# Performance work log

Measured on AMD Instinct MI355X. Metric: run time of the kernel, lower is better.

Reference implementation:

```python
import jax, jax.numpy as jnp
import numpy as np

N_POINTS = 4
HIDDEN = 128


def _grid_sample(features, grid):
    """Bilinear grid_sample, align_corners=True, zero padding.
    features: [B, C, H, W]; grid: [B, J, P, 2] with (x, y) in [-1, 1].
    Returns [B, C, J, P]."""
    B, C, H, W = features.shape
    ix = (grid[..., 0] + 1.0) * 0.5 * (W - 1)  # [B,J,P]
    iy = (grid[..., 1] + 1.0) * 0.5 * (H - 1)
    x0 = jnp.floor(ix); y0 = jnp.floor(iy)
    x1 = x0 + 1.0;      y1 = y0 + 1.0
    wx1 = ix - x0; wx0 = 1.0 - wx1
    wy1 = iy - y0; wy0 = 1.0 - wy1

    def corner(xf, yf):
        valid = (xf >= 0) & (xf <= W - 1) & (yf >= 0) & (yf <= H - 1)
        xi = jnp.clip(xf, 0, W - 1).astype(jnp.int32)
        yi = jnp.clip(yf, 0, H - 1).astype(jnp.int32)

        def gather_one(fb, yb, xb, vb):
            # fb: [C,H,W]; yb, xb, vb: [J,P]
            return fb[:, yb, xb] * vb[None].astype(fb.dtype)  # [C,J,P]

        return jax.vmap(gather_one)(features, yi, xi, valid)

    v00 = corner(x0, y0); v01 = corner(x1, y0)
    v10 = corner(x0, y1); v11 = corner(x1, y1)
    w00 = (wx0 * wy0)[:, None]  # [B,1,J,P]
    w01 = (wx1 * wy0)[:, None]
    w10 = (wx0 * wy1)[:, None]
    w11 = (wx1 * wy1)[:, None]
    return v00 * w00 + v01 * w01 + v10 * w10 + v11 * w11


def _mlp1x1(x, w1, b1, w2, b2):
    # 1x1 conv stack on [B, C, J] points: Conv(C->128) -> ReLU -> Conv(128->O)
    h = jax.nn.relu(jnp.einsum('oc,bcj->boj', w1, x) + b1[None, :, None])
    return jnp.einsum('oc,bcj->boj', w2, h) + b2[None, :, None]


def setup_inputs() -> dict:
    key = jax.random.key(0)
    ks = jax.random.split(key, 12)
    B, C, H, W, J = 32, 1024, 64, 64, 128
    features = jax.random.normal(ks[0], (B, C, H, W), dtype=jnp.float32)
    keypoint_coords = jax.random.uniform(ks[1], (B, J, 2), dtype=jnp.float32,
                                         minval=-1.0, maxval=1.0)
    # offset predictor params (small std so predicted pixel offsets stay local)
    w_off1 = jax.random.normal(ks[2], (HIDDEN, C), dtype=jnp.float32) * 0.01
    b_off1 = jax.random.normal(ks[3], (HIDDEN,), dtype=jnp.float32) * 0.01
    w_off2 = jax.random.normal(ks[4], (2 * N_POINTS, HIDDEN), dtype=jnp.float32) * 0.01
    b_off2 = jax.random.normal(ks[5], (2 * N_POINTS,), dtype=jnp.float32) * 0.01
    # attention predictor params
    w_att1 = jax.random.normal(ks[6], (HIDDEN, C), dtype=jnp.float32) * 0.02
    b_att1 = jax.random.normal(ks[7], (HIDDEN,), dtype=jnp.float32) * 0.02
    w_att2 = jax.random.normal(ks[8], (N_POINTS, HIDDEN), dtype=jnp.float32) * 0.02
    b_att2 = jax.random.normal(ks[9], (N_POINTS,), dtype=jnp.float32) * 0.02
    return {"features": features, "keypoint_coords": keypoint_coords,
            "w_off1": w_off1, "b_off1": b_off1, "w_off2": w_off2, "b_off2": b_off2,
            "w_att1": w_att1, "b_att1": b_att1, "w_att2": w_att2, "b_att2": b_att2}


def reference(features, keypoint_coords, w_off1, b_off1, w_off2, b_off2,
              w_att1, b_att1, w_att2, b_att2):
    B, C, H, W = features.shape
    J = keypoint_coords.shape[1]
    # seed features at keypoints: [B, C, J]
    seed = _grid_sample(features, keypoint_coords[:, :, None, :])[..., 0]
    offsets = _mlp1x1(seed, w_off1, b_off1, w_off2, b_off2)      # [B, 2N, J]
    attn_logits = _mlp1x1(seed, w_att1, b_att1, w_att2, b_att2)  # [B, N, J]
    # [B, 2N, J] -> [B, J, N, 2]; channel pairs are (x, y) per point
    off = offsets.transpose(0, 2, 1).reshape(B, J, N_POINTS, 2)
    scale = jnp.array([2.0 / (W - 1), 2.0 / (H - 1)], dtype=features.dtype)
    new_grid = keypoint_coords[:, :, None, :] + off * scale       # [B, J, N, 2]
    sampled = _grid_sample(features, new_grid)                    # [B, C, J, N]
    attw = jax.nn.softmax(attn_logits.transpose(0, 2, 1), axis=-1)  # [B, J, N]
    fused = jnp.einsum('bcjn,bjn->bjc', sampled, attw)            # [B, J, C]
    return fused
```

## Files before the change

kernel.cpp:

```cpp
#include <hip/hip_runtime.h>
#include <math.h>

#define BB  32
#define CCH 1024
#define HH  64
#define WW  64
#define JJ  128
#define NP  4
#define HID 128

typedef float f4 __attribute__((ext_vector_type(4)));
typedef __attribute__((ext_vector_type(8))) short bf8_t;
typedef __attribute__((ext_vector_type(4))) float f32x4;
typedef __attribute__((ext_vector_type(4))) unsigned short us4;

__device__ __forceinline__ unsigned short f2bf(float x) {
  union { float f; unsigned int u; } v; v.f = x;
  unsigned int u = v.u;
  return (unsigned short)((u + 0x7FFFu + ((u >> 16) & 1u)) >> 16);
}

__device__ __forceinline__ float bilin(const float* pl, float ix, float iy) {
  float x0f = floorf(ix), y0f = floorf(iy);
  float wx1 = ix - x0f, wx0 = 1.0f - wx1;
  float wy1 = iy - y0f, wy0 = 1.0f - wy1;
  int x0 = (int)x0f, y0 = (int)y0f;
  int x1 = x0 + 1, y1 = y0 + 1;
  float v = 0.0f;
  if (y0 >= 0 && y0 < HH) {
    if (x0 >= 0 && x0 < WW) v += pl[y0*WW + x0] * (wx0*wy0);
    if (x1 >= 0 && x1 < WW) v += pl[y0*WW + x1] * (wx1*wy0);
  }
  if (y1 >= 0 && y1 < HH) {
    if (x0 >= 0 && x0 < WW) v += pl[y1*WW + x0] * (wx0*wy1);
    if (x1 >= 0 && x1 < WW) v += pl[y1*WW + x1] * (wx1*wy1);
  }
  return v;
}

__global__ __launch_bounds__(256) void k_prep(const float* __restrict__ w_off1,
                                              const float* __restrict__ w_att1,
                                              unsigned short* __restrict__ Wb) {
  int o = blockIdx.x, m = blockIdx.y;
  const float* src = (m ? w_att1 : w_off1) + (size_t)o * CCH;
  unsigned short* dst = Wb + ((size_t)m * HID + o) * CCH;
  int t = threadIdx.x;
  f4 v = *(const f4*)&src[t * 4];
  us4 u; u[0] = f2bf(v[0]); u[1] = f2bf(v[1]); u[2] = f2bf(v[2]); u[3] = f2bf(v[3]);
  *(us4*)&dst[t * 4] = u;
}

__global__ __launch_bounds__(256) void k_seed(const float* __restrict__ feat,
                                              const float* __restrict__ kp,
                                              unsigned short* __restrict__ seedB) {
  int c = blockIdx.x, b = blockIdx.y;
  __shared__ __align__(16) float pl[HH*WW];
  const f4* p4 = (const f4*)(feat + ((size_t)(b*CCH + c)) * (size_t)(HH*WW));
  f4* s4 = (f4*)pl;
  #pragma unroll
  for (int r = 0; r < 4; ++r) s4[threadIdx.x + r*256] = p4[threadIdx.x + r*256];
  __syncthreads();
  int j = threadIdx.x;
  if (j < JJ) {
    float gx = kp[((size_t)b*JJ + j)*2 + 0];
    float gy = kp[((size_t)b*JJ + j)*2 + 1];
    float ix = (gx + 1.0f) * 0.5f * (float)(WW - 1);
    float iy = (gy + 1.0f) * 0.5f * (float)(HH - 1);
    seedB[((size_t)(b*CCH + c))*JJ + j] = f2bf(bilin(pl, ix, iy));
  }
}

__global__ __launch_bounds__(256) void k_str(const unsigned short* __restrict__ seedB,
                                             unsigned short* __restrict__ seedT) {
  int c0 = blockIdx.x * 32, j0 = blockIdx.y * 32, b = blockIdx.z;
  __shared__ unsigned short tl[32][34];
  int tx = threadIdx.x & 31, ty = threadIdx.x >> 5;
  #pragma unroll
  for (int r = 0; r < 4; ++r)
    tl[ty + r*8][tx] = seedB[((size_t)(b*CCH + c0 + ty + r*8))*JJ + j0 + tx];
  __syncthreads();
  #pragma unroll
  for (int r = 0; r < 4; ++r) {
    int jr = ty + r*8;
    seedT[((size_t)b*JJ + j0 + jr)*CCH + c0 + tx] = tl[tx][jr];
  }
}

__global__ __launch_bounds__(256) void k_mlp2(const unsigned short* __restrict__ seedT,
                                              const unsigned short* __restrict__ Wb,
                                              const float* __restrict__ b_off1,
                                              const float* __restrict__ b_att1,
                                              float* __restrict__ hidden) {
  int m = blockIdx.x, b = blockIdx.y;
  __shared__ __align__(16) unsigned short sA[128][72];
  __shared__ __align__(16) unsigned short sB[128][72];
  int t = threadIdx.x;
  int w = t >> 6, l = t & 63;
  int lr = l & 15, lg = l >> 4;
  f32x4 acc[2][8];
  #pragma unroll
  for (int jt = 0; jt < 2; ++jt)
    #pragma unroll
    for (int ot = 0; ot < 8; ++ot) acc[jt][ot] = (f32x4)0.0f;

  const unsigned short* At = seedT + (size_t)b * JJ * CCH;
  const unsigned short* Bt = Wb + (size_t)m * HID * CCH;

  for (int kc = 0; kc < 16; ++kc) {
    int k0 = kc * 64;
    #pragma unroll
    for (int q = 0; q < 4; ++q) {
      int idx = q * 256 + t;
      int r = idx >> 3, s = idx & 7;
      *(bf8_t*)&sA[r][s*8] = *(const bf8_t*)&At[(size_t)r*CCH + k0 + s*8];
      *(bf8_t*)&sB[r][s*8] = *(const bf8_t*)&Bt[(size_t)r*CCH + k0 + s*8];
    }
    __syncthreads();
    #pragma unroll
    for (int ks = 0; ks < 2; ++ks) {
      int koff = ks*32 + lg*8;
      bf8_t a0 = *(const bf8_t*)&sA[w*32 + lr][koff];
      bf8_t a1 = *(const bf8_t*)&sA[w*32 + 16 + lr][koff];
      #pragma unroll
      for (int ot = 0; ot < 8; ++ot) {
        bf8_t bb = *(const bf8_t*)&sB[ot*16 + lr][koff];
        acc[0][ot] = __builtin_amdgcn_mfma_f32_16x16x32_bf16(a0, bb, acc[0][ot], 0, 0, 0);
        acc[1][ot] = __builtin_amdgcn_mfma_f32_16x16x32_bf16(a1, bb, acc[1][ot], 0, 0, 0);
      }
    }
    __syncthreads();
  }

  const float* bias = m ? b_att1 : b_off1;
  float* Hb = hidden + ((size_t)b * 2 + m) * JJ * HID;
  #pragma unroll
  for (int jt = 0; jt < 2; ++jt) {
    #pragma unroll
    for (int ot = 0; ot < 8; ++ot) {
      int o = ot*16 + lr;
      float bo = bias[o];
      #pragma unroll
      for (int r = 0; r < 4; ++r) {
        int j = w*32 + jt*16 + lg*4 + r;
        Hb[(size_t)j*HID + o] = fmaxf(acc[jt][ot][r] + bo, 0.0f);
      }
    }
  }
}

__global__ __launch_bounds__(256) void k_head2(const float* __restrict__ hidden,
                                               const float* __restrict__ kp,
                                               const float* __restrict__ w_off2,
                                               const float* __restrict__ b_off2,
                                               const float* __restrict__ w_att2,
                                               const float* __restrict__ b_att2,
                                               float* __restrict__ grids,
                                               float* __restrict__ attw) {
  int jq = blockIdx.x, b = blockIdx.y;
  int j0 = jq * 32;
  __shared__ __align__(16) float sH[2][32][132];
  __shared__ float sO[32][13];
  int t = threadIdx.x;
  for (int idx = t; idx < 2048; idx += 256) {
    int m = idx >> 10, rem = idx & 1023;
    int jl = rem >> 5, oq = rem & 31;
    *(f4*)&sH[m][jl][oq*4] =
        *(const f4*)&hidden[(((size_t)b*2 + m)*JJ + j0 + jl)*HID + oq*4];
  }
  __syncthreads();
  for (int idx = t; idx < 12*32; idx += 256) {
    int jl = idx / 12, q = idx % 12;
    int m = (q < 8) ? 0 : 1;
    int p = m ? (q - 8) : q;
    const float* w2 = m ? w_att2 : w_off2;
    float sum = (m ? b_att2 : b_off2)[p];
    for (int o = 0; o < HID; ++o) sum += w2[p*HID + o] * sH[m][jl][o];
    sO[jl][q] = sum;
  }
  __syncthreads();
  if (t < 32) {
    int jl = t, j = j0 + jl;
    float gx = kp[((size_t)b*JJ + j)*2 + 0];
    float gy = kp[((size_t)b*JJ + j)*2 + 1];
    const float sc = 2.0f / 63.0f;
    float a[NP];
    #pragma unroll
    for (int n = 0; n < NP; ++n) {
      grids[(((size_t)b*JJ + j)*NP + n)*2 + 0] = gx + sO[jl][2*n + 0]*sc;
      grids[(((size_t)b*JJ + j)*NP + n)*2 + 1] = gy + sO[jl][2*n + 1]*sc;
      a[n] = sO[jl][8 + n];
    }
    float mx = fmaxf(fmaxf(a[0], a[1]), fmaxf(a[2], a[3]));
    float e[NP], s = 0.0f;
    #pragma unroll
    for (int n = 0; n < NP; ++n) { e[n] = expf(a[n] - mx); s += e[n]; }
    float inv = 1.0f / s;
    #pragma unroll
    for (int n = 0; n < NP; ++n) attw[((size_t)b*JJ + j)*NP + n] = e[n]*inv;
  }
}

__global__ __launch_bounds__(256) void k_fuse2(const float* __restrict__ feat,
                                               const float* __restrict__ grids,
                                               const float* __restrict__ attw,
                                               float* __restrict__ out) {
  int c0 = blockIdx.x * 16;
  int b = (BB - 1) - blockIdx.y;
  __shared__ __align__(16) float plane[2][HH*WW];
  __shared__ float sT[JJ][17];
  __shared__ float sG[JJ*NP*2];
  __shared__ float sAw[JJ*NP];
  int t = threadIdx.x;
  const f4* gb = (const f4*)(grids + (size_t)b*JJ*NP*2);
  const f4* ab = (const f4*)(attw  + (size_t)b*JJ*NP);
  ((f4*)sG)[t] = gb[t];
  if (t < 128) ((f4*)sAw)[t] = ab[t];

  const float* base = feat + ((size_t)(b*CCH + c0)) * (size_t)(HH*WW);
  f4 r[4];
  {
    const f4* p0 = (const f4*)base;
    #pragma unroll
    for (int q = 0; q < 4; ++q) r[q] = p0[t + q*256];
    f4* d = (f4*)plane[0];
    #pragma unroll
    for (int q = 0; q < 4; ++q) d[t + q*256] = r[q];
  }
  __syncthreads();

  for (int i = 0; i < 16; ++i) {
    int cur = i & 1;
    if (i < 15) {
      const f4* pn = (const f4*)(base + (size_t)(i + 1) * (HH*WW));
      #pragma unroll
      for (int q = 0; q < 4; ++q) r[q] = pn[t + q*256];
    }
    if (t < JJ) {
      float acc = 0.0f;
      #pragma unroll
      for (int n = 0; n < NP; ++n) {
        float gx = sG[(t*NP + n)*2 + 0];
        float gy = sG[(t*NP + n)*2 + 1];
        float ix = (gx + 1.0f) * 0.5f * (float)(WW - 1);
        float iy = (gy + 1.0f) * 0.5f * (float)(HH - 1);
        acc += sAw[t*NP + n] * bilin(plane[cur], ix, iy);
      }
      sT[t][i] = acc;
    }
    __syncthreads();
    if (i < 15) {
      f4* d = (f4*)plane[cur ^ 1];
      #pragma unroll
      for (int q = 0; q < 4; ++q) d[t + q*256] = r[q];
    }
    __syncthreads();
  }

  if (t < JJ) {
    f4* dst = (f4*)&out[((size_t)b*JJ + t)*CCH + c0];
    #pragma unroll
    for (int q = 0; q < 4; ++q) {
      f4 v;
      v[0] = sT[t][q*4 + 0]; v[1] = sT[t][q*4 + 1];
      v[2] = sT[t][q*4 + 2]; v[3] = sT[t][q*4 + 3];
      dst[q] = v;
    }
  }
}

extern "C" void kernel_launch(void* const* d_in, const int* in_sizes, int n_in,
                              void* d_out, int out_size, void* d_ws, size_t ws_size,
                              hipStream_t stream) {
  const float* feat   = (const float*)d_in[0];
  const float* kp     = (const float*)d_in[1];
  const float* w_off1 = (const float*)d_in[2];
  const float* b_off1 = (const float*)d_in[3];
  const float* w_off2 = (const float*)d_in[4];
  const float* b_off2 = (const float*)d_in[5];
  const float* w_att1 = (const float*)d_in[6];
  const float* b_att1 = (const float*)d_in[7];
  const float* w_att2 = (const float*)d_in[8];
  const float* b_att2 = (const float*)d_in[9];
  float* out = (float*)d_out;

  float* ws = (float*)d_ws;
  float*          grids = ws;
  float*          attwb = ws + (size_t)32768;
  unsigned short* Wb    = (unsigned short*)(ws + (size_t)49152);
  unsigned short* seedB = (unsigned short*)(ws + (size_t)180224);
  unsigned short* seedT = (unsigned short*)(ws + (size_t)2277376);
  float*          hid   = ws + (size_t)4374528;

  k_prep <<<dim3(HID, 2), 256, 0, stream>>>(w_off1, w_att1, Wb);
  k_seed <<<dim3(CCH, BB), 256, 0, stream>>>(feat, kp, seedB);
  k_str  <<<dim3(CCH/32, JJ/32, BB), 256, 0, stream>>>(seedB, seedT);
  k_mlp2 <<<dim3(2, BB), 256, 0, stream>>>(seedT, Wb, b_off1, b_att1, hid);
  k_head2<<<dim3(4, BB), 256, 0, stream>>>(hid, kp, w_off2, b_off2, w_att2, b_att2,
                                           grids, attwb);
  k_fuse2<<<dim3(CCH/16, BB), 256, 0, stream>>>(feat, grids, attwb, out);
}
```

Baseline: 232.4 us.

## Fuse second MLP layer and softmax into hidden-layer GEMM kernel, split J

Merges the head kernel into the first-layer MFMA GEMM kernel. The hidden activations stay in shared memory and the grids and attention weights are written directly, so the global hidden buffer and one kernel launch go away. The GEMM grid is also split over two halves of J, doubling the block count from 64 to 128 to raise occupancy. In exchange the weight tile is reloaded by twice as many blocks, and each block uses more shared memory.

```diff
diff --git a/kernel.cpp b/kernel.cpp
--- a/kernel.cpp
+++ b/kernel.cpp
@@ -86,117 +86,116 @@
   }
 }
 
-__global__ __launch_bounds__(256) void k_mlp2(const unsigned short* __restrict__ seedT,
+__global__ __launch_bounds__(256) void k_mlp3(const unsigned short* __restrict__ seedT,
                                               const unsigned short* __restrict__ Wb,
                                               const float* __restrict__ b_off1,
                                               const float* __restrict__ b_att1,
-                                              float* __restrict__ hidden) {
-  int m = blockIdx.x, b = blockIdx.y;
-  __shared__ __align__(16) unsigned short sA[128][72];
+                                              const float* __restrict__ kp,
+                                              const float* __restrict__ w_off2,
+                                              const float* __restrict__ b_off2,
+                                              const float* __restrict__ w_att2,
+                                              const float* __restrict__ b_att2,
+                                              float* __restrict__ grids,
+                                              float* __restrict__ attw) {
+  int m = blockIdx.x, jh = blockIdx.y, b = blockIdx.z;
+  __shared__ __align__(16) unsigned short sA[64][72];
   __shared__ __align__(16) unsigned short sB[128][72];
+  __shared__ __align__(16) float sH[64][132];
+  __shared__ float sO[64][13];
   int t = threadIdx.x;
   int w = t >> 6, l = t & 63;
   int lr = l & 15, lg = l >> 4;
-  f32x4 acc[2][8];
-  #pragma unroll
-  for (int jt = 0; jt < 2; ++jt)
-    #pragma unroll
-    for (int ot = 0; ot < 8; ++ot) acc[jt][ot] = (f32x4)0.0f;
-
-  const unsigned short* At = seedT + (size_t)b * JJ * CCH;
+  f32x4 acc[8];
+  #pragma unroll
+  for (int ot = 0; ot < 8; ++ot) acc[ot] = (f32x4)0.0f;
+
+  const unsigned short* At = seedT + ((size_t)b * JJ + jh * 64) * CCH;
   const unsigned short* Bt = Wb + (size_t)m * HID * CCH;
 
   for (int kc = 0; kc < 16; ++kc) {
     int k0 = kc * 64;
+    #pragma unroll
+    for (int q = 0; q < 2; ++q) {
+      int idx = q * 256 + t;
+      int r = idx >> 3, s = idx & 7;
+      *(bf8_t*)&sA[r][s*8] = *(const bf8_t*)&At[(size_t)r*CCH + k0 + s*8];
+    }
     #pragma unroll
     for (int q = 0; q < 4; ++q) {
       int idx = q * 256 + t;
       int r = idx >> 3, s = idx & 7;
-      *(bf8_t*)&sA[r][s*8] = *(const bf8_t*)&At[(size_t)r*CCH + k0 + s*8];
       *(bf8_t*)&sB[r][s*8] = *(const bf8_t*)&Bt[(size_t)r*CCH + k0 + s*8];
     }
     __syncthreads();
     #pragma unroll
     for (int ks = 0; ks < 2; ++ks) {
       int koff = ks*32 + lg*8;
-      bf8_t a0 = *(const bf8_t*)&sA[w*32 + lr][koff];
-      bf8_t a1 = *(const bf8_t*)&sA[w*32 + 16 + lr][koff];
+      bf8_t a0 = *(const bf8_t*)&sA[w*16 + lr][koff];
       #pragma unroll
       for (int ot = 0; ot < 8; ++ot) {
         bf8_t bb = *(const bf8_t*)&sB[ot*16 + lr][koff];
-        acc[0][ot] = __builtin_amdgcn_mfma_f32_16x16x32_bf16(a0, bb, acc[0][ot], 0, 0, 0);
-        acc[1][ot] = __builtin_amdgcn_mfma_f32_16x16x32_bf16(a1, bb, acc[1][ot], 0, 0, 0);
+        acc[ot] = __builtin_amdgcn_mfma_f32_16x16x32_bf16(a0, bb, acc[ot], 0, 0, 0);
       }
     }
     __syncthreads();
   }
 
   const float* bias = m ? b_att1 : b_off1;
-  float* Hb = hidden + ((size_t)b * 2 + m) * JJ * HID;
-  #pragma unroll
-  for (int jt = 0; jt < 2; ++jt) {
-    #pragma unroll
-    for (int ot = 0; ot < 8; ++ot) {
-      int o = ot*16 + lr;
-      float bo = bias[o];
-      #pragma unroll
-      for (int r = 0; r < 4; ++r) {
-        int j = w*32 + jt*16 + lg*4 + r;
-        Hb[(size_t)j*HID + o] = fmaxf(acc[jt][ot][r] + bo, 0.0f);
+  #pragma unroll
+  for (int ot = 0; ot < 8; ++ot) {
+    int o = ot*16 + lr;
+    float bo = bias[o];
+    #pragma unroll
+    for (int r = 0; r < 4; ++r) {
+      int jl = w*16 + lg*4 + r;
+      sH[jl][o] = fmaxf(acc[ot][r] + bo, 0.0f);
+    }
+  }
+  __syncthreads();
+
+  if (m == 0) {
+    for (int idx = t; idx < 64*8; idx += 256) {
+      int jl = idx >> 3, p = idx & 7;
+      const float* w2 = w_off2 + (size_t)p * HID;
+      float sum = b_off2[p];
+      #pragma unroll 8
+      for (int o = 0; o < HID; ++o) sum += w2[o] * sH[jl][o];
+      sO[jl][p] = sum;
+    }
+  } else {
+    for (int idx = t; idx < 64*4; idx += 256) {
+      int jl = idx >> 2, p = idx & 3;
+      const float* w2 = w_att2 + (size_t)p * HID;
+      float sum = b_att2[p];
+      #pragma unroll 8
+      for (int o = 0; o < HID; ++o) sum += w2[o] * sH[jl][o];
+      sO[jl][p] = sum;
+    }
+  }
+  __syncthreads();
+
+  if (t < 64) {
+    int j = jh*64 + t;
+    if (m == 0) {
+      float gx = kp[((size_t)b*JJ + j)*2 + 0];
+      float gy = kp[((size_t)b*JJ + j)*2 + 1];
+      const float sc = 2.0f / 63.0f;
+      #pragma unroll
+      for (int n = 0; n < NP; ++n) {
+        grids[(((size_t)b*JJ + j)*NP + n)*2 + 0] = gx + sO[t][2*n + 0]*sc;
+        grids[(((size_t)b*JJ + j)*NP + n)*2 + 1] = gy + sO[t][2*n + 1]*sc;
       }
-    }
-  }
-}
-
-__global__ __launch_bounds__(256) void k_head2(const float* __restrict__ hidden,
-                                               const float* __restrict__ kp,
-                                               const float* __restrict__ w_off2,
-                                               const float* __restrict__ b_off2,
-                                               const float* __restrict__ w_att2,
-                                               const float* __restrict__ b_att2,
-                                               float* __restrict__ grids,
-                                               float* __restrict__ attw) {
-  int jq = blockIdx.x, b = blockIdx.y;
-  int j0 = jq * 32;
-  __shared__ __align__(16) float sH[2][32][132];
-  __shared__ float sO[32][13];
-  int t = threadIdx.x;
-  for (int idx = t; idx < 2048; idx += 256) {
-    int m = idx >> 10, rem = idx & 1023;
-    int jl = rem >> 5, oq = rem & 31;
-    *(f4*)&sH[m][jl][oq*4] =
-        *(const f4*)&hidden[(((size_t)b*2 + m)*JJ + j0 + jl)*HID + oq*4];
-  }
-  __syncthreads();
-  for (int idx = t; idx < 12*32; idx += 256) {
-    int jl = idx / 12, q = idx % 12;
-    int m = (q < 8) ? 0 : 1;
-    int p = m ? (q - 8) : q;
-    const float* w2 = m ? w_att2 : w_off2;
-    float sum = (m ? b_att2 : b_off2)[p];
-    for (int o = 0; o < HID; ++o) sum += w2[p*HID + o] * sH[m][jl][o];
-    sO[jl][q] = sum;
-  }
-  __syncthreads();
-  if (t < 32) {
-    int jl = t, j = j0 + jl;
-    float gx = kp[((size_t)b*JJ + j)*2 + 0];
-    float gy = kp[((size_t)b*JJ + j)*2 + 1];
-    const float sc = 2.0f / 63.0f;
-    float a[NP];
-    #pragma unroll
-    for (int n = 0; n < NP; ++n) {
-      grids[(((size_t)b*JJ + j)*NP + n)*2 + 0] = gx + sO[jl][2*n + 0]*sc;
-      grids[(((size_t)b*JJ + j)*NP + n)*2 + 1] = gy + sO[jl][2*n + 1]*sc;
-      a[n] = sO[jl][8 + n];
-    }
-    float mx = fmaxf(fmaxf(a[0], a[1]), fmaxf(a[2], a[3]));
-    float e[NP], s = 0.0f;
-    #pragma unroll
-    for (int n = 0; n < NP; ++n) { e[n] = expf(a[n] - mx); s += e[n]; }
-    float inv = 1.0f / s;
-    #pragma unroll
-    for (int n = 0; n < NP; ++n) attw[((size_t)b*JJ + j)*NP + n] = e[n]*inv;
+    } else {
+      float a0 = sO[t][0], a1 = sO[t][1], a2 = sO[t][2], a3 = sO[t][3];
+      float mx = fmaxf(fmaxf(a0, a1), fmaxf(a2, a3));
+      float e0 = expf(a0 - mx), e1 = expf(a1 - mx);
+      float e2 = expf(a2 - mx), e3 = expf(a3 - mx);
+      float inv = 1.0f / (e0 + e1 + e2 + e3);
+      attw[((size_t)b*JJ + j)*NP + 0] = e0*inv;
+      attw[((size_t)b*JJ + j)*NP + 1] = e1*inv;
+      attw[((size_t)b*JJ + j)*NP + 2] = e2*inv;
+      attw[((size_t)b*JJ + j)*NP + 3] = e3*inv;
+    }
   }
 }
 
@@ -289,13 +288,12 @@
   unsigned short* Wb    = (unsigned short*)(ws + (size_t)49152);
   unsigned short* seedB = (unsigned short*)(ws + (size_t)180224);
   unsigned short* seedT = (unsigned short*)(ws + (size_t)2277376);
-  float*          hid   = ws + (size_t)4374528;
 
   k_prep <<<dim3(HID, 2), 256, 0, stream>>>(w_off1, w_att1, Wb);
   k_seed <<<dim3(CCH, BB), 256, 0, stream>>>(feat, kp, seedB);
   k_str  <<<dim3(CCH/32, JJ/32, BB), 256, 0, stream>>>(seedB, seedT);
-  k_mlp2 <<<dim3(2, BB), 256, 0, stream>>>(seedT, Wb, b_off1, b_att1, hid);
-  k_head2<<<dim3(4, BB), 256, 0, stream>>>(hid, kp, w_off2, b_off2, w_att2, b_att2,
-                                           grids, attwb);
+  k_mlp3 <<<dim3(2, 2, BB), 256, 0, stream>>>(seedT, Wb, b_off1, b_att1, kp,
+                                              w_off2, b_off2, w_att2, b_att2,
+                                              grids, attwb);
   k_fuse2<<<dim3(CCH/16, BB), 256, 0, stream>>>(feat, grids, attwb, out);
 }
```

Result: faster. 225.4 us (-3.0%).
